# Performance work log

Hardware: AMD Instinct MI355X
Metric: run time of the kernel (lower is better)

The kernel has to match this reference:

```python
import jax, jax.numpy as jnp
import numpy as np

DT = 0.01        # base_dt from __init__
DT_SCALE = 1.0   # forward default


def setup_inputs() -> dict:
    key = jax.random.key(0)
    k1, k2, k3, k4, k5 = jax.random.split(key, 5)
    B, D, R = 4096, 512, 128
    x = jax.random.normal(k1, (B, D), dtype=jnp.float32)
    v = jax.random.normal(k2, (B, D), dtype=jnp.float32)
    force = jax.random.normal(k3, (B, D), dtype=jnp.float32)
    U = jax.random.normal(k4, (D, R), dtype=jnp.float32) * (1.0 / np.sqrt(D))
    W = jax.random.normal(k5, (R, D), dtype=jnp.float32) * (1.0 / np.sqrt(R))
    return {"x": x, "v": v, "force": force, "U": U, "W": W, "steps": 8}


def reference(x, v, force, U, W, steps):
    dt = DT * DT_SCALE
    # Dormand-Prince (DP5) tableau
    a21 = 1/5
    a31, a32 = 3/40, 9/40
    a41, a42, a43 = 44/45, -56/15, 32/9
    a51, a52, a53, a54 = 19372/6561, -25360/2187, 64448/6561, -212/729
    a61, a62, a63, a64, a65 = 9017/3168, -355/33, 46732/5247, 49/176, -5103/18656
    b1, b3, b4, b5, b6 = 35/384, 500/1113, 125/192, -2187/6784, 11/84

    def dynamics(tx, tv):
        # low-rank Christoffel: gamma(v, x) = ((v @ U) * (x @ U)) @ W
        acc = -jnp.einsum('br,rd->bd', (tv @ U) * (tx @ U), W)
        return acc + force

    def step(carry, _):
        cx, cv = carry
        k1x = cv
        k1v = dynamics(cx, cv)
        x2 = cx + dt * (a21 * k1x); v2 = cv + dt * (a21 * k1v)
        k2x = v2; k2v = dynamics(x2, v2)
        x3 = cx + dt * (a31 * k1x + a32 * k2x)
        v3 = cv + dt * (a31 * k1v + a32 * k2v)
        k3x = v3; k3v = dynamics(x3, v3)
        x4 = cx + dt * (a41 * k1x + a42 * k2x + a43 * k3x)
        v4 = cv + dt * (a41 * k1v + a42 * k2v + a43 * k3v)
        k4x = v4; k4v = dynamics(x4, v4)
        x5 = cx + dt * (a51 * k1x + a52 * k2x + a53 * k3x + a54 * k4x)
        v5 = cv + dt * (a51 * k1v + a52 * k2v + a53 * k3v + a54 * k4v)
        k5x = v5; k5v = dynamics(x5, v5)
        x6 = cx + dt * (a61 * k1x + a62 * k2x + a63 * k3x + a64 * k4x + a65 * k5x)
        v6 = cv + dt * (a61 * k1v + a62 * k2v + a63 * k3v + a64 * k4v + a65 * k5v)
        k6x = v6; k6v = dynamics(x6, v6)
        nx = cx + dt * (b1 * k1x + b3 * k3x + b4 * k4x + b5 * k5x + b6 * k6x)
        nv = cv + dt * (b1 * k1v + b3 * k3v + b4 * k4v + b5 * k5v + b6 * k6v)
        return (nx, nv), None

    (fx, fv), _ = jax.lax.scan(step, (x, v), None, length=steps)
    return fx, fv
```

## Files before the change

kernel.cpp:

```cpp
#include <hip/hip_runtime.h>


typedef _Float16 v8h __attribute__((ext_vector_type(8)));
typedef float v4f __attribute__((ext_vector_type(4)));
typedef unsigned short u16;
typedef unsigned int u32;

#define MFMAH __builtin_amdgcn_mfma_f32_16x16x32_f16
#define INV2048 4.8828125e-4f
#define INV256  0.00390625f
#define SSTR 144

__device__ __forceinline__ float swap8(float x){
  return __int_as_float(
    __builtin_amdgcn_mov_dpp(__float_as_int(x), 0x128, 0xf, 0xf, true));
}

struct Tab {
  double a[7][7]; double b[7]; double A[7]; double XC[7][7]; double XF[7]; double cxc[7];
};
static constexpr Tab make_tab() {
  Tab t{};
  t.a[2][1]=1.0/5;
  t.a[3][1]=3.0/40;       t.a[3][2]=9.0/40;
  t.a[4][1]=44.0/45;      t.a[4][2]=-56.0/15;      t.a[4][3]=32.0/9;
  t.a[5][1]=19372.0/6561; t.a[5][2]=-25360.0/2187; t.a[5][3]=64448.0/6561; t.a[5][4]=-212.0/729;
  t.a[6][1]=9017.0/3168;  t.a[6][2]=-355.0/33;     t.a[6][3]=46732.0/5247; t.a[6][4]=49.0/176; t.a[6][5]=-5103.0/18656;
  t.b[1]=35.0/384; t.b[2]=0.0; t.b[3]=500.0/1113; t.b[4]=125.0/192; t.b[5]=-2187.0/6784; t.b[6]=11.0/84;
  for (int i=1;i<=6;++i){ double s=0; for(int j=1;j<i;++j) s+=t.a[i][j]; t.A[i]=s; }
  for (int i=1;i<=6;++i) for(int l=1;l<i;++l){ double s=0; for(int j=l+1;j<i;++j) s+=t.a[i][j]*t.a[j][l]; t.XC[i][l]=s; }
  for (int i=1;i<=6;++i){ double s=0; for(int j=1;j<i;++j) s+=t.a[i][j]*t.A[j]; t.XF[i]=s; }
  for (int j=1;j<=6;++j){ double s=0; for (int i=j+1;i<=6;++i) s+=t.b[i]*t.a[i][j]; t.cxc[j]=s; }
  return t;
}
static constexpr Tab TB = make_tab();

__device__ __forceinline__ int decode_steps(const void* p){
  int v = *(const int*)p;
  if (v >= 1 && v <= 512) return v;
  float f = *(const float*)p;
  if (f >= 1.f && f <= 512.f) return (int)f;
  return 8;
}
__device__ __forceinline__ void split2s(float x, _Float16& h, _Float16& l){
  h = (_Float16)x;
  l = (_Float16)((x - (float)h) * 2048.0f);
}

#define WS_GH 0
#define WS_GL 16384
#define WS_UH 32768
#define WS_UL 98304
#define WS_WH 163840
#define WS_WL 229376

__global__ __launch_bounds__(512) void k_prep(const float* __restrict__ Ug,
                                              const float* __restrict__ Wg,
                                              _Float16* __restrict__ ws){
  const int tid = threadIdx.x;
  if (blockIdx.x >= 8) {
    int t = (blockIdx.x - 8)*512 + tid;
    if (t < 65536) {
      int r = t >> 7, c = t & 127;
      _Float16 h, l; split2s(Ug[t]*256.f, h, l);
      int kb=r>>5, q2=(r>>3)&3, j=r&7, n2=c>>4, cl=c&15;
      int slot = ((n2*16+kb)*64 + q2*16+cl)*8 + j;
      ws[WS_UH + slot] = h; ws[WS_UL + slot] = l;
    } else {
      int idx = t - 65536;
      int r = idx >> 9, c = idx & 511;
      _Float16 h, l; split2s(Wg[idx]*256.f, h, l);
      int kb=r>>5, q2=(r>>3)&3, j=r&7, n2=c>>4, cl=c&15;
      int slot = ((n2*4+kb)*64 + q2*16+cl)*8 + j;
      ws[WS_WH + slot] = h; ws[WS_WL + slot] = l;
    }
  } else {
    const int b = blockIdx.x;
    const int ww = tid >> 6, lane = tid & 63, q = lane >> 4, c16 = lane & 15;
    const int nb = ww;
    v4f aH = {0,0,0,0}, aC0 = {0,0,0,0}, aC1 = {0,0,0,0};
    #pragma unroll
    for (int kb = 0; kb < 16; ++kb) {
      const float* wp = Wg + (b*16 + c16)*512 + kb*32 + q*8;
      float4 w0 = *(const float4*)wp;
      float4 w1 = *(const float4*)(wp + 4);
      float wv[8] = {w0.x,w0.y,w0.z,w0.w, w1.x,w1.y,w1.z,w1.w};
      v8h Ah, Al, Bh, Bl;
      #pragma unroll
      for (int j = 0; j < 8; ++j) {
        _Float16 h, l; split2s(-wv[j], h, l);
        Ah[j] = h; Al[j] = l;
        float uv = Ug[(kb*32 + q*8 + j)*128 + nb*16 + c16] * 256.f;
        split2s(uv, h, l);
        Bh[j] = h; Bl[j] = l;
      }
      aH = MFMAH(Ah, Bh, aH, 0,0,0);
      if (kb & 1) {
        aC1 = MFMAH(Ah, Bl, aC1, 0,0,0);
        aC1 = MFMAH(Al, Bh, aC1, 0,0,0);
      } else {
        aC0 = MFMAH(Ah, Bl, aC0, 0,0,0);
        aC0 = MFMAH(Al, Bh, aC0, 0,0,0);
      }
    }
    #pragma unroll
    for (int r = 0; r < 4; ++r) {
      float g = aH[r] + (aC0[r] + aC1[r])*INV2048;
      _Float16 h, l; split2s(g, h, l);
      int m = b*16 + 4*q + r, n = nb*16 + c16;
      int slot = (((n>>4)*4 + (m>>5))*64 + ((m>>3)&3)*16 + (n&15))*8 + (m&7);
      ws[WS_GH + slot] = h; ws[WS_GL + slot] = l;
    }
  }
}

#define ARENA 33280

__global__ __launch_bounds__(512,4) void dp5_main(
    const float* __restrict__ xg, const float* __restrict__ vg,
    const float* __restrict__ fg, const void* stepsp,
    const _Float16* __restrict__ ws, float* __restrict__ outg)
{
  __shared__ __align__(16) char arena[ARENA];
  _Float16* base = (_Float16*)arena;
  const _Float16* uH = ws + WS_UH;
  const _Float16* uL = ws + WS_UL;
  const _Float16* wH = ws + WS_WH;
  const _Float16* wL = ws + WS_WL;

  const int tid  = threadIdx.x;
  const int ww   = tid >> 6;
  const int lane = tid & 63;
  const int q    = lane >> 4;
  const int c16  = lane & 15;
  const int nb   = ww;
  const int kcol = nb*16 + c16;
  const int srcl = (q>>1)*16 + c16;
  const bool odd = (q & 1);
  const int rb   = blockIdx.x * 8;
  const int S    = decode_steps(stepsp);
  const float dt = 0.01f;
  const int  brow = c16 & 7;
  const bool hiC  = (c16 >= 8);
  const int  kc0  = nb*16 + 4*q + (hiC ? 2 : 0);

  v8h Gh[4], Gl[4];
  #pragma unroll
  for (int kb = 0; kb < 4; ++kb) {
    int off = ((nb*4 + kb)*64 + lane)*8;
    Gh[kb] = *(const v8h*)(ws + WS_GH + off);
    Gl[kb] = *(const v8h*)(ws + WS_GL + off);
  }

  _Float16* tH = base;
  _Float16* tL = base + 8320;
  const int r16 = tid >> 5, c0 = (tid & 31)*16;
  float xU0[2], vU0[2], fU0[2];
  for (int pass = 0; pass < 2; ++pass) {
    if (pass == 0 || r16 < 8) {
      const float* sp;
      if (pass == 0) sp = (r16 < 8) ? (xg + (rb + r16)*512) : (vg + (rb + r16 - 8)*512);
      else           sp = fg + (rb + r16)*512;
      sp += c0;
      float4 g0 = *(const float4*)(sp);
      float4 g1 = *(const float4*)(sp + 4);
      float4 g2 = *(const float4*)(sp + 8);
      float4 g3 = *(const float4*)(sp + 12);
      float vals[16] = {g0.x,g0.y,g0.z,g0.w, g1.x,g1.y,g1.z,g1.w,
                        g2.x,g2.y,g2.z,g2.w, g3.x,g3.y,g3.z,g3.w};
      v8h vh0, vh1, vl0, vl1;
      #pragma unroll
      for (int j = 0; j < 8; ++j) {
        _Float16 h, l;
        split2s(vals[j], h, l);     vh0[j] = h; vl0[j] = l;
        split2s(vals[8+j], h, l);   vh1[j] = h; vl1[j] = l;
      }
      int o = r16*520 + c0;
      *(v8h*)(tH + o) = vh0; *(v8h*)(tH + o + 8) = vh1;
      *(v8h*)(tL + o) = vl0; *(v8h*)(tL + o + 8) = vl1;
    }
    __syncthreads();
    v4f aH0={0,0,0,0}, aH1={0,0,0,0}, aC0={0,0,0,0}, aC1={0,0,0,0};
    #pragma unroll
    for (int kb = 0; kb < 16; ++kb) {
      int ao = c16*520 + kb*32 + q*8;
      v8h Ah = *(const v8h*)(tH + ao);
      v8h Al = *(const v8h*)(tL + ao);
      int bo = ((nb*16 + kb)*64 + lane)*8;
      v8h Bh = *(const v8h*)(uH + bo);
      v8h Bl = *(const v8h*)(uL + bo);
      if (kb & 1) {
        aH1 = MFMAH(Ah, Bh, aH1, 0,0,0);
        aC1 = MFMAH(Ah, Bl, aC1, 0,0,0);
        aC1 = MFMAH(Al, Bh, aC1, 0,0,0);
      } else {
        aH0 = MFMAH(Ah, Bh, aH0, 0,0,0);
        aC0 = MFMAH(Ah, Bl, aC0, 0,0,0);
        aC0 = MFMAH(Al, Bh, aC0, 0,0,0);
      }
    }
    float at0 = ((aH0[0]+aH1[0]) + (aC0[0]+aC1[0])*INV2048)*INV256;
    float at1 = ((aH0[1]+aH1[1]) + (aC0[1]+aC1[1])*INV2048)*INV256;
    float at2 = ((aH0[2]+aH1[2]) + (aC0[2]+aC1[2])*INV2048)*INV256;
    float at3 = ((aH0[3]+aH1[3]) + (aC0[3]+aC1[3])*INV2048)*INV256;
    if (pass == 0) {
      float sx0=__shfl(at0,srcl,64), sx1=__shfl(at1,srcl,64);
      float sx2=__shfl(at2,srcl,64), sx3=__shfl(at3,srcl,64);
      xU0[0] = odd ? sx2 : sx0; xU0[1] = odd ? sx3 : sx1;
      int srclv = srcl + 32;
      float sv0=__shfl(at0,srclv,64), sv1=__shfl(at1,srclv,64);
      float sv2=__shfl(at2,srclv,64), sv3=__shfl(at3,srclv,64);
      vU0[0] = odd ? sv2 : sv0; vU0[1] = odd ? sv3 : sv1;
    } else {
      float sf0=__shfl(at0,srcl,64), sf1=__shfl(at1,srcl,64);
      float sf2=__shfl(at2,srcl,64), sf3=__shfl(at3,srcl,64);
      fU0[0] = odd ? sf2 : sf0; fU0[1] = odd ? sf3 : sf1;
    }
    __syncthreads();
  }

  float cxU2[2], cvU2[2], fU2[2];
  {
    float* T = (float*)arena;
    #pragma unroll
    for (int p2 = 0; p2 < 3; ++p2) {
      float i0 = (p2==0) ? xU0[0] : (p2==1) ? vU0[0] : fU0[0];
      float i1 = (p2==0) ? xU0[1] : (p2==1) ? vU0[1] : fU0[1];
      T[(2*q + 0)*132 + kcol] = i0;
      T[(2*q + 1)*132 + kcol] = i1;
      __syncthreads();
      float2 t2 = *(const float2*)(T + brow*132 + kc0);
      float* o = (p2==0) ? cxU2 : (p2==1) ? cvU2 : fU2;
      o[0] = t2.x; o[1] = t2.y;
      __syncthreads();
    }
  }

  float kU6[6][2], Rr2[2], QXa2[2];
  #pragma unroll
  for (int j = 0; j < 2; ++j) {
    Rr2[j] = 0.f; QXa2[j] = 0.f;
    #pragma unroll
    for (int l = 0; l < 6; ++l) kU6[l][j] = 0.f;
  }

  int pb = 0;
  for (int s = 0; s < S; ++s) {
    float accX[2], accV[2], Pbs[2], Pxcs[2];
    #pragma unroll
    for (int j = 0; j < 2; ++j) { accX[j]=0.f; accV[j]=0.f; Pbs[j]=0.f; Pxcs[j]=0.f; }

    #pragma unroll
    for (int i = 1; i <= 6; ++i) {
      _Float16* bT = base + (pb ? 2304 : 0);
      const float dtA   = dt*(float)TB.A[i];
      const float dt2XF = dt*dt*(float)TB.XF[i];
      const float bi    = (float)TB.b[i];
      const float ci    = (float)TB.cxc[i];
      {
        union { _Float16 h[2]; u32 u; } ph, pl;
        #pragma unroll
        for (int j2 = 0; j2 < 2; ++j2) {
          float vv = cvU2[j2] + dtA*fU2[j2];
          float xx = cxU2[j2] + dtA*cvU2[j2] + dt2XF*fU2[j2];
          #pragma unroll
          for (int l = 1; l < i; ++l) {
            vv += (dt*(float)TB.a[i][l]) * kU6[l-1][j2];
            xx += (dt*dt*(float)TB.XC[i][l]) * kU6[l-1][j2];
          }
          float p = vv*xx;
          Pbs[j2] += bi*p; Pxcs[j2] += ci*p;
          _Float16 h, l2; split2s(p, h, l2);
          ph.h[j2] = h; pl.h[j2] = l2;
        }
        *(u32*)(bT + brow*SSTR + kc0)       = ph.u;
        *(u32*)(bT + (8+brow)*SSTR + kc0)   = pl.u;
      }
      __syncthreads();
      v4f C1 = {0,0,0,0}, C2 = {0,0,0,0};
      #pragma unroll
      for (int kb = 0; kb < 4; ++kb) {
        v8h B = *(const v8h*)(bT + c16*SSTR + kb*32 + q*8);
        C1 = MFMAH(Gh[kb], B, C1, 0,0,0);
        C2 = MFMAH(Gl[kb], B, C2, 0,0,0);
      }
      float kv[4];
      #pragma unroll
      for (int r = 0; r < 4; ++r) {
        float oth = swap8(C1[r]);
        kv[r] = (C1[r] + (oth + C2[r])*INV2048)*INV256;
      }
      float k2 = swap8(kv[2]);
      float k3 = swap8(kv[3]);
      float kva = hiC ? k2 : kv[0];
      float kvb = hiC ? k3 : kv[1];
      kU6[i-1][0] = kva; kU6[i-1][1] = kvb;
      accX[0] += ci*kva; accV[0] += bi*kva;
      accX[1] += ci*kvb; accV[1] += bi*kvb;
      pb ^= 1;
    }

    #pragma unroll
    for (int j = 0; j < 2; ++j) {
      float nx = cxU2[j] + dt*cvU2[j] + dt*dt*(accX[j] + 0.5f*fU2[j]);
      cvU2[j] += dt*(accV[j] + fU2[j]);
      cxU2[j]  = nx;
      QXa2[j] += Rr2[j] + Pxcs[j];
      Rr2[j]  += Pbs[j];
    }
  }

  __syncthreads();
  _Float16* RQh = base;
  _Float16* RQl = base + 2176;
  {
    union { _Float16 h[2]; u32 u; } t1, t2, t3, t4;
    #pragma unroll
    for (int j2 = 0; j2 < 2; ++j2) {
      _Float16 h, l;
      split2s(Rr2[j2], h, l);  t1.h[j2] = h; t2.h[j2] = l;
      split2s(QXa2[j2], h, l); t3.h[j2] = h; t4.h[j2] = l;
    }
    *(u32*)(RQh + brow*136 + kc0)     = t1.u;
    *(u32*)(RQl + brow*136 + kc0)     = t2.u;
    *(u32*)(RQh + (8+brow)*136 + kc0) = t3.u;
    *(u32*)(RQl + (8+brow)*136 + kc0) = t4.u;
  }
  __syncthreads();

  const float Sdt = (float)S * dt;
  #pragma unroll
  for (int cbi = 0; cbi < 4; ++cbi) {
    int cb = nb*4 + cbi;
    v4f aH={0,0,0,0}, aC0={0,0,0,0}, aC1={0,0,0,0};
    #pragma unroll
    for (int kb = 0; kb < 4; ++kb) {
      int bo = ((cb*4 + kb)*64 + lane)*8;
      v8h Bh = *(const v8h*)(wH + bo);
      v8h Bl = *(const v8h*)(wL + bo);
      int ao = c16*136 + kb*32 + q*8;
      v8h Ah = *(const v8h*)(RQh + ao);
      v8h Al = *(const v8h*)(RQl + ao);
      aH = MFMAH(Ah, Bh, aH, 0,0,0);
      if (kb & 1) {
        aC1 = MFMAH(Ah, Bl, aC1, 0,0,0);
        aC1 = MFMAH(Al, Bh, aC1, 0,0,0);
      } else {
        aC0 = MFMAH(Ah, Bl, aC0, 0,0,0);
        aC0 = MFMAH(Al, Bh, aC0, 0,0,0);
      }
    }
    float r0 = (aH[0] + (aC0[0]+aC1[0])*INV2048)*INV256;
    float r1 = (aH[1] + (aC0[1]+aC1[1])*INV2048)*INV256;
    float r2 = (aH[2] + (aC0[2]+aC1[2])*INV2048)*INV256;
    float r3 = (aH[3] + (aC0[3]+aC1[3])*INV2048)*INV256;
    float o0 = __shfl_xor(r0, 32, 64);
    float o1 = __shfl_xor(r1, 32, 64);
    float o2 = __shfl_xor(r2, 32, 64);
    float o3 = __shfl_xor(r3, 32, 64);
    if (q < 2) {
      float abv[4] = {r0, r1, r2, r3};
      float axv[4] = {o0, o1, o2, o3};
      #pragma unroll
      for (int i4 = 0; i4 < 4; ++i4) {
        int off = (rb + 4*q + i4)*512 + cb*16 + c16;
        float x0 = xg[off], v0 = vg[off], f0 = fg[off];
        outg[off]           = x0 + Sdt*v0 + 0.5f*Sdt*Sdt*f0 - dt*dt*axv[i4];
        outg[2097152 + off] = v0 + Sdt*f0 - dt*abv[i4];
      }
    }
  }
}

extern "C" void kernel_launch(void* const* d_in, const int* in_sizes, int n_in,
                              void* d_out, int out_size, void* d_ws, size_t ws_size,
                              hipStream_t stream) {
  const float* x = (const float*)d_in[0];
  const float* v = (const float*)d_in[1];
  const float* f = (const float*)d_in[2];
  const float* U = (const float*)d_in[3];
  const float* W = (const float*)d_in[4];
  _Float16* ws = (_Float16*)d_ws;

  k_prep<<<dim3(264), dim3(512), 0, stream>>>(U, W, ws);
  dp5_main<<<dim3(512), dim3(512), 0, stream>>>(
      x, v, f, d_in[5], ws, (float*)d_out);
}
```

Before: 145.7 us.

## Fuse force projection into single pass and vectorize output epilogue via LDS staging

Loads x, v and force rows into LDS at once and runs both projection GEMMs in one k-loop, removing the second pass and its barriers. The final output step stages the per-row corrections in LDS, then reads x/v/f and writes both outputs as coalesced float4 instead of scattered scalar accesses. It also hoists the B-fragment LDS loads ahead of the MFMA chain. The arena grows to about 49 KB, which may limit how many blocks fit per CU.

```diff
diff --git a/kernel.cpp b/kernel.cpp
--- a/kernel.cpp
+++ b/kernel.cpp
@@ -114,7 +114,7 @@
   }
 }
 
-#define ARENA 33280
+#define ARENA 49920
 
 __global__ __launch_bounds__(512,4) void dp5_main(
     const float* __restrict__ xg, const float* __restrict__ vg,
@@ -153,14 +153,12 @@
   }
 
   _Float16* tH = base;
-  _Float16* tL = base + 8320;
+  _Float16* tL = base + 12480;
   const int r16 = tid >> 5, c0 = (tid & 31)*16;
   float xU0[2], vU0[2], fU0[2];
-  for (int pass = 0; pass < 2; ++pass) {
-    if (pass == 0 || r16 < 8) {
-      const float* sp;
-      if (pass == 0) sp = (r16 < 8) ? (xg + (rb + r16)*512) : (vg + (rb + r16 - 8)*512);
-      else           sp = fg + (rb + r16)*512;
+  {
+    {
+      const float* sp = (r16 < 8) ? (xg + (rb + r16)*512) : (vg + (rb + r16 - 8)*512);
       sp += c0;
       float4 g0 = *(const float4*)(sp);
       float4 g1 = *(const float4*)(sp + 4);
@@ -179,31 +177,66 @@
       *(v8h*)(tH + o) = vh0; *(v8h*)(tH + o + 8) = vh1;
       *(v8h*)(tL + o) = vl0; *(v8h*)(tL + o + 8) = vl1;
     }
+    if (r16 < 8) {
+      const float* sp = fg + (rb + r16)*512 + c0;
+      float4 g0 = *(const float4*)(sp);
+      float4 g1 = *(const float4*)(sp + 4);
+      float4 g2 = *(const float4*)(sp + 8);
+      float4 g3 = *(const float4*)(sp + 12);
+      float vals[16] = {g0.x,g0.y,g0.z,g0.w, g1.x,g1.y,g1.z,g1.w,
+                        g2.x,g2.y,g2.z,g2.w, g3.x,g3.y,g3.z,g3.w};
+      v8h vh0, vh1, vl0, vl1;
+      #pragma unroll
+      for (int j = 0; j < 8; ++j) {
+        _Float16 h, l;
+        split2s(vals[j], h, l);     vh0[j] = h; vl0[j] = l;
+        split2s(vals[8+j], h, l);   vh1[j] = h; vl1[j] = l;
+      }
+      int o = (16 + r16)*520 + c0;
+      *(v8h*)(tH + o) = vh0; *(v8h*)(tH + o + 8) = vh1;
+      *(v8h*)(tL + o) = vl0; *(v8h*)(tL + o + 8) = vl1;
+    }
     __syncthreads();
+
     v4f aH0={0,0,0,0}, aH1={0,0,0,0}, aC0={0,0,0,0}, aC1={0,0,0,0};
+    v4f bH0={0,0,0,0}, bH1={0,0,0,0}, bC0={0,0,0,0}, bC1={0,0,0,0};
+    const int arow1 = (c16 < 8) ? (16 + c16) : c16;
     #pragma unroll
     for (int kb = 0; kb < 16; ++kb) {
-      int ao = c16*520 + kb*32 + q*8;
-      v8h Ah = *(const v8h*)(tH + ao);
-      v8h Al = *(const v8h*)(tL + ao);
+      int ao0 = c16*520 + kb*32 + q*8;
+      int ao1 = arow1*520 + kb*32 + q*8;
+      v8h Ah0 = *(const v8h*)(tH + ao0);
+      v8h Al0 = *(const v8h*)(tL + ao0);
+      v8h Ah1 = *(const v8h*)(tH + ao1);
+      v8h Al1 = *(const v8h*)(tL + ao1);
       int bo = ((nb*16 + kb)*64 + lane)*8;
       v8h Bh = *(const v8h*)(uH + bo);
       v8h Bl = *(const v8h*)(uL + bo);
       if (kb & 1) {
-        aH1 = MFMAH(Ah, Bh, aH1, 0,0,0);
-        aC1 = MFMAH(Ah, Bl, aC1, 0,0,0);
-        aC1 = MFMAH(Al, Bh, aC1, 0,0,0);
+        aH1 = MFMAH(Ah0, Bh, aH1, 0,0,0);
+        aC1 = MFMAH(Ah0, Bl, aC1, 0,0,0);
+        aC1 = MFMAH(Al0, Bh, aC1, 0,0,0);
+        bH1 = MFMAH(Ah1, Bh, bH1, 0,0,0);
+        bC1 = MFMAH(Ah1, Bl, bC1, 0,0,0);
+        bC1 = MFMAH(Al1, Bh, bC1, 0,0,0);
       } else {
-        aH0 = MFMAH(Ah, Bh, aH0, 0,0,0);
-        aC0 = MFMAH(Ah, Bl, aC0, 0,0,0);
-        aC0 = MFMAH(Al, Bh, aC0, 0,0,0);
+        aH0 = MFMAH(Ah0, Bh, aH0, 0,0,0);
+        aC0 = MFMAH(Ah0, Bl, aC0, 0,0,0);
+        aC0 = MFMAH(Al0, Bh, aC0, 0,0,0);
+        bH0 = MFMAH(Ah1, Bh, bH0, 0,0,0);
+        bC0 = MFMAH(Ah1, Bl, bC0, 0,0,0);
+        bC0 = MFMAH(Al1, Bh, bC0, 0,0,0);
       }
     }
     float at0 = ((aH0[0]+aH1[0]) + (aC0[0]+aC1[0])*INV2048)*INV256;
     float at1 = ((aH0[1]+aH1[1]) + (aC0[1]+aC1[1])*INV2048)*INV256;
     float at2 = ((aH0[2]+aH1[2]) + (aC0[2]+aC1[2])*INV2048)*INV256;
     float at3 = ((aH0[3]+aH1[3]) + (aC0[3]+aC1[3])*INV2048)*INV256;
-    if (pass == 0) {
+    float bt0 = ((bH0[0]+bH1[0]) + (bC0[0]+bC1[0])*INV2048)*INV256;
+    float bt1 = ((bH0[1]+bH1[1]) + (bC0[1]+bC1[1])*INV2048)*INV256;
+    float bt2 = ((bH0[2]+bH1[2]) + (bC0[2]+bC1[2])*INV2048)*INV256;
+    float bt3 = ((bH0[3]+bH1[3]) + (bC0[3]+bC1[3])*INV2048)*INV256;
+    {
       float sx0=__shfl(at0,srcl,64), sx1=__shfl(at1,srcl,64);
       float sx2=__shfl(at2,srcl,64), sx3=__shfl(at3,srcl,64);
       xU0[0] = odd ? sx2 : sx0; xU0[1] = odd ? sx3 : sx1;
@@ -211,9 +244,10 @@
       float sv0=__shfl(at0,srclv,64), sv1=__shfl(at1,srclv,64);
       float sv2=__shfl(at2,srclv,64), sv3=__shfl(at3,srclv,64);
       vU0[0] = odd ? sv2 : sv0; vU0[1] = odd ? sv3 : sv1;
-    } else {
-      float sf0=__shfl(at0,srcl,64), sf1=__shfl(at1,srcl,64);
-      float sf2=__shfl(at2,srcl,64), sf3=__shfl(at3,srcl,64);
+    }
+    {
+      float sf0=__shfl(bt0,srcl,64), sf1=__shfl(bt1,srcl,64);
+      float sf2=__shfl(bt2,srcl,64), sf3=__shfl(bt3,srcl,64);
       fU0[0] = odd ? sf2 : sf0; fU0[1] = odd ? sf3 : sf1;
     }
     __syncthreads();
@@ -277,13 +311,16 @@
         *(u32*)(bT + (8+brow)*SSTR + kc0)   = pl.u;
       }
       __syncthreads();
+      const _Float16* bp = bT + c16*SSTR + q*8;
+      v8h B0 = *(const v8h*)(bp);
+      v8h B1 = *(const v8h*)(bp + 32);
+      v8h B2 = *(const v8h*)(bp + 64);
+      v8h B3 = *(const v8h*)(bp + 96);
       v4f C1 = {0,0,0,0}, C2 = {0,0,0,0};
-      #pragma unroll
-      for (int kb = 0; kb < 4; ++kb) {
-        v8h B = *(const v8h*)(bT + c16*SSTR + kb*32 + q*8);
-        C1 = MFMAH(Gh[kb], B, C1, 0,0,0);
-        C2 = MFMAH(Gl[kb], B, C2, 0,0,0);
-      }
+      C1 = MFMAH(Gh[0], B0, C1, 0,0,0);  C2 = MFMAH(Gl[0], B0, C2, 0,0,0);
+      C1 = MFMAH(Gh[1], B1, C1, 0,0,0);  C2 = MFMAH(Gl[1], B1, C2, 0,0,0);
+      C1 = MFMAH(Gh[2], B2, C1, 0,0,0);  C2 = MFMAH(Gl[2], B2, C2, 0,0,0);
+      C1 = MFMAH(Gh[3], B3, C1, 0,0,0);  C2 = MFMAH(Gl[3], B3, C2, 0,0,0);
       float kv[4];
       #pragma unroll
       for (int r = 0; r < 4; ++r) {
@@ -328,7 +365,9 @@
   }
   __syncthreads();
 
-  const float Sdt = (float)S * dt;
+  float* axs = (float*)(arena + 9216);
+  float* abs_ = (float*)(arena + 25600);
+
   #pragma unroll
   for (int cbi = 0; cbi < 4; ++cbi) {
     int cb = nb*4 + cbi;
@@ -363,12 +402,38 @@
       float axv[4] = {o0, o1, o2, o3};
       #pragma unroll
       for (int i4 = 0; i4 < 4; ++i4) {
-        int off = (rb + 4*q + i4)*512 + cb*16 + c16;
-        float x0 = xg[off], v0 = vg[off], f0 = fg[off];
-        outg[off]           = x0 + Sdt*v0 + 0.5f*Sdt*Sdt*f0 - dt*dt*axv[i4];
-        outg[2097152 + off] = v0 + Sdt*f0 - dt*abv[i4];
-      }
-    }
+        int lrow = 4*q + i4;
+        int lcol = cb*16 + c16;
+        axs[lrow*512 + lcol]  = axv[i4];
+        abs_[lrow*512 + lcol] = abv[i4];
+      }
+    }
+  }
+  __syncthreads();
+
+  const float Sdt = (float)S * dt;
+  #pragma unroll
+  for (int half = 0; half < 2; ++half) {
+    int flat = half*2048 + tid*4;
+    int row  = flat >> 9;
+    int col  = flat & 511;
+    int go   = (rb + row)*512 + col;
+    float4 xv = *(const float4*)(xg + go);
+    float4 vv = *(const float4*)(vg + go);
+    float4 fv = *(const float4*)(fg + go);
+    float4 axf = *(const float4*)(axs + flat);
+    float4 abf = *(const float4*)(abs_ + flat);
+    float4 o1, o2;
+    o1.x = xv.x + Sdt*vv.x + 0.5f*Sdt*Sdt*fv.x - dt*dt*axf.x;
+    o1.y = xv.y + Sdt*vv.y + 0.5f*Sdt*Sdt*fv.y - dt*dt*axf.y;
+    o1.z = xv.z + Sdt*vv.z + 0.5f*Sdt*Sdt*fv.z - dt*dt*axf.z;
+    o1.w = xv.w + Sdt*vv.w + 0.5f*Sdt*Sdt*fv.w - dt*dt*axf.w;
+    o2.x = vv.x + Sdt*fv.x - dt*abf.x;
+    o2.y = vv.y + Sdt*fv.y - dt*abf.y;
+    o2.z = vv.z + Sdt*fv.z - dt*abf.z;
+    o2.w = vv.w + Sdt*fv.w - dt*abf.w;
+    *(float4*)(outg + go) = o1;
+    *(float4*)(outg + 2097152 + go) = o2;
   }
 }
 
```

After: 136.4 us. 6.4% less time.
